# Kernel optimization log

Hardware: AMD Instinct MI355X
Metric: run time of the kernel (lower is better)

## Reference

```python
import jax, jax.numpy as jnp
import numpy as np

ROWS, COLS, P = 64, 64, 32
Q = 10                 # num_classes
TAU_EFF = 7
T1 = TAU_EFF + 1       # time bins
WRES = 3
WMAX = 2 ** WRES - 1   # 7
N = ROWS * COLS * P    # 131072 voter inputs


def setup_inputs() -> dict:
    key = jax.random.key(0)
    k_sp, _ = jax.random.split(key)
    # spike times in [0, tau_eff+2]; values >= tau_eff get clamped in forward
    input_spikes = jax.random.randint(k_sp, (ROWS, COLS, P), 0, TAU_EFF + 3).astype(jnp.float32)
    # w_init='half' -> wmax/2 everywhere
    weights = (WMAX / 2) * jnp.ones((2, N, Q, T1), dtype=jnp.float32)
    return {"input_spikes": input_spikes, "weights": weights}


def reference(input_spikes, weights):
    # flatten spikes: (rows, cols, p) -> (N,)
    v = input_spikes.reshape(-1)
    # clamp finite spike times >= tau_eff to tau_eff (Inf stays Inf)
    v = jnp.where((v >= TAU_EFF) & (v != jnp.inf), jnp.float32(TAU_EFF), v)
    # one-hot over time bins: equals torch's (const - voter_in) nonzero->-1, +1 trick.
    # Inf spike times produce all-zero rows (const - inf = -inf != 0), matching torch.
    const = jnp.arange(T1, dtype=jnp.float32)                       # (T1,)
    onehot = (const[None, None, None, :] == v[None, :, None, None]) # (2-broadcast later)
    voter_in = jnp.broadcast_to(onehot, (2, N, Q, T1)).astype(jnp.float32)
    # select weights at the spike-time bin; vote where selected weight >= wmax/2
    sel_weights = voter_in * weights                                # (2, N, Q, T1)
    votes = (sel_weights >= WMAX / 2).astype(jnp.float32)           # (2, N, Q, T1)
    # tally per class: sum over polarity, neurons, time bins
    tally = votes.sum(axis=(0, 1, 3))                               # (Q,)
    prediction = jnp.zeros((Q,), jnp.float32).at[jnp.argmax(tally)].set(1.0)
    return prediction, voter_in[0], votes
```

## Files before the change

### kernel.cpp

```cpp
#include <hip/hip_runtime.h>
#include <math.h>

#define NN      131072
#define Q       10
#define T1      8
#define GRID    2048
#define BLOCK   256

#define VIN0_OFF   10u
#define VIN0_SZ    (NN * Q * T1)
#define VOTES_OFF  (VIN0_OFF + VIN0_SZ)
#define VOTES_SZ   (2u * NN * Q * T1)
#define E_F2       (VOTES_SZ / 2u)

__global__ __launch_bounds__(BLOCK) void dtnn_main(
    const float* __restrict__ spikes,
    const float* __restrict__ weights,
    float* __restrict__ out,
    unsigned int* __restrict__ tallies)
{
    const unsigned int lane = threadIdx.x & 63u;
    const unsigned int wid  = threadIdx.x >> 6;

    float2* __restrict__ votes2 = (float2*)(out + VOTES_OFF);
    float2* __restrict__ vin2   = (float2*)(out + VIN0_OFF);

    unsigned int acc = 0u;

    const unsigned int stride = GRID * BLOCK;
    for (unsigned int j = blockIdx.x * BLOCK + threadIdx.x; j < E_F2; j += stride) {
        const unsigned int r    = j >> 2;
        const unsigned int slot = j & 3u;
        const unsigned int ri   = r / Q;
        const unsigned int q    = r - Q * ri;
        const unsigned int i    = ri & (NN - 1u);

        float v = spikes[i];
        v = (v >= 7.0f && !isinf(v)) ? 7.0f : v;
        const float t0 = (float)(2u * slot);
        const bool  h0 = (v == t0);
        const bool  h1 = (v == t0 + 1.0f);

        int tv = (int)v;
        tv = tv < 0 ? 0 : (tv > 7 ? 7 : tv);
        const float w  = weights[r * 8u + (unsigned)tv];
        const bool  gw = (w >= 3.5f);

        const float vx = (h0 && gw) ? 1.0f : 0.0f;
        const float vy = (h1 && gw) ? 1.0f : 0.0f;
        votes2[j] = make_float2(vx, vy);

        if (r < NN * Q) {
            vin2[j] = make_float2(h0 ? 1.0f : 0.0f, h1 ? 1.0f : 0.0f);
        }

        const bool inc = (vx != 0.0f) | (vy != 0.0f);
        #pragma unroll
        for (int k = 0; k < Q; ++k) {
            const unsigned long long m = __ballot(inc && (q == (unsigned)k));
            if (lane == (unsigned)k) acc += (unsigned)__popcll(m);
        }
    }

    __shared__ unsigned int lt[4 * Q];
    if (lane < Q) lt[wid * Q + lane] = acc;
    __syncthreads();
    if (threadIdx.x < Q) {
        tallies[threadIdx.x * GRID + blockIdx.x] =
            lt[threadIdx.x] + lt[Q + threadIdx.x] + lt[2 * Q + threadIdx.x] + lt[3 * Q + threadIdx.x];
    }
}

__global__ __launch_bounds__(64 * Q) void dtnn_pred(
    const unsigned int* __restrict__ tallies,
    float* __restrict__ out)
{
    const unsigned int lane = threadIdx.x & 63u;
    const unsigned int q    = threadIdx.x >> 6;

    unsigned int s = 0;
    #pragma unroll
    for (int it = 0; it < GRID / 64; ++it)
        s += tallies[q * GRID + it * 64 + lane];
    #pragma unroll
    for (int off = 32; off >= 1; off >>= 1)
        s += __shfl_down(s, off, 64);

    __shared__ unsigned int sums[Q];
    if (lane == 0) sums[q] = s;
    __syncthreads();

    if (threadIdx.x == 0) {
        unsigned int best = sums[0]; int bi = 0;
        #pragma unroll
        for (int k = 1; k < Q; ++k)
            if (sums[k] > best) { best = sums[k]; bi = k; }
        #pragma unroll
        for (int k = 0; k < Q; ++k) out[k] = (k == bi) ? 1.0f : 0.0f;
    }
}

extern "C" void kernel_launch(void* const* d_in, const int* in_sizes, int n_in,
                              void* d_out, int out_size, void* d_ws, size_t ws_size,
                              hipStream_t stream) {
    const float* spikes  = (const float*)d_in[0];
    const float* weights = (const float*)d_in[1];
    float* out = (float*)d_out;
    unsigned int* tallies = (unsigned int*)d_ws;

    dtnn_main<<<GRID, BLOCK, 0, stream>>>(spikes, weights, out, tallies);
    dtnn_pred<<<1, 64 * Q, 0, stream>>>(tallies, out);
}
```

Measured before the change: 43.87 us.

## Split vote computation into bitmask pass and separate output-writing pass

The fused kernel is split in two. The first pass does one gather per (polarity, neuron, class) row, packs the vote bits into a 64-bit ballot mask in workspace, and accumulates tallies. The second pass reads the compact mask to write the votes and voter_in arrays, using contiguous per-block chunks instead of a grid-stride loop. The goal is to take the scattered weight reads out of the store-bound output loop, at the cost of an extra kernel launch and a round trip of the mask through workspace.

```diff
diff --git a/kernel.cpp b/kernel.cpp
--- a/kernel.cpp
+++ b/kernel.cpp
@@ -12,53 +12,50 @@
 #define VOTES_OFF  (VIN0_OFF + VIN0_SZ)
 #define VOTES_SZ   (2u * NN * Q * T1)
 #define E_F2       (VOTES_SZ / 2u)
+#define CHUNK2     (E_F2 / GRID)
 
-__global__ __launch_bounds__(BLOCK) void dtnn_main(
+#define ROWS_T     (2u * NN * Q)
+#define CHUNK1     (ROWS_T / GRID)
+#define MASK_WORDS (ROWS_T / 64u)
+
+#define TALLY_BYTES (Q * GRID * 4)
+
+__global__ __launch_bounds__(BLOCK) void dtnn_pass1(
     const float* __restrict__ spikes,
     const float* __restrict__ weights,
-    float* __restrict__ out,
+    unsigned long long* __restrict__ mask,
     unsigned int* __restrict__ tallies)
 {
     const unsigned int lane = threadIdx.x & 63u;
     const unsigned int wid  = threadIdx.x >> 6;
 
-    float2* __restrict__ votes2 = (float2*)(out + VOTES_OFF);
-    float2* __restrict__ vin2   = (float2*)(out + VIN0_OFF);
-
     unsigned int acc = 0u;
 
-    const unsigned int stride = GRID * BLOCK;
-    for (unsigned int j = blockIdx.x * BLOCK + threadIdx.x; j < E_F2; j += stride) {
-        const unsigned int r    = j >> 2;
-        const unsigned int slot = j & 3u;
-        const unsigned int ri   = r / Q;
-        const unsigned int q    = r - Q * ri;
-        const unsigned int i    = ri & (NN - 1u);
+    const unsigned int row_base = blockIdx.x * CHUNK1 + threadIdx.x;
+    #pragma unroll 1
+    for (unsigned int it = 0; it < CHUNK1 / BLOCK; ++it) {
+        const unsigned int row = row_base + it * BLOCK;
+        const unsigned int ri  = row / Q;
+        const unsigned int q   = row - Q * ri;
+        const unsigned int i   = ri & (NN - 1u);
 
         float v = spikes[i];
-        v = (v >= 7.0f && !isinf(v)) ? 7.0f : v;
-        const float t0 = (float)(2u * slot);
-        const bool  h0 = (v == t0);
-        const bool  h1 = (v == t0 + 1.0f);
+        if (v >= 7.0f && !isinf(v)) v = 7.0f;
+        const int  tv    = (int)v;
+        const bool valid = (v >= 0.0f) && (v < 8.0f) && ((float)tv == v);
 
-        int tv = (int)v;
-        tv = tv < 0 ? 0 : (tv > 7 ? 7 : tv);
-        const float w  = weights[r * 8u + (unsigned)tv];
-        const bool  gw = (w >= 3.5f);
-
-        const float vx = (h0 && gw) ? 1.0f : 0.0f;
-        const float vy = (h1 && gw) ? 1.0f : 0.0f;
-        votes2[j] = make_float2(vx, vy);
-
-        if (r < NN * Q) {
-            vin2[j] = make_float2(h0 ? 1.0f : 0.0f, h1 ? 1.0f : 0.0f);
+        bool vote = false;
+        if (valid) {
+            vote = (weights[row * 8u + (unsigned)tv] >= 3.5f);
         }
 
-        const bool inc = (vx != 0.0f) | (vy != 0.0f);
+        const unsigned long long m = __ballot(vote);
+        if (lane == 0) mask[row >> 6] = m;
+
         #pragma unroll
         for (int k = 0; k < Q; ++k) {
-            const unsigned long long m = __ballot(inc && (q == (unsigned)k));
-            if (lane == (unsigned)k) acc += (unsigned)__popcll(m);
+            const unsigned long long mk = __ballot(vote && (q == (unsigned)k));
+            if (lane == (unsigned)k) acc += (unsigned)__popcll(mk);
         }
     }
 
@@ -68,6 +65,40 @@
     if (threadIdx.x < Q) {
         tallies[threadIdx.x * GRID + blockIdx.x] =
             lt[threadIdx.x] + lt[Q + threadIdx.x] + lt[2 * Q + threadIdx.x] + lt[3 * Q + threadIdx.x];
+    }
+}
+
+__global__ __launch_bounds__(BLOCK) void dtnn_pass2(
+    const float* __restrict__ spikes,
+    const unsigned long long* __restrict__ mask,
+    float* __restrict__ out)
+{
+    float2* __restrict__ votes2 = (float2*)(out + VOTES_OFF);
+    float2* __restrict__ vin2   = (float2*)(out + VIN0_OFF);
+
+    const unsigned int jbase = blockIdx.x * CHUNK2 + threadIdx.x;
+    #pragma unroll 1
+    for (unsigned int it = 0; it < CHUNK2 / BLOCK; ++it) {
+        const unsigned int j    = jbase + it * BLOCK;
+        const unsigned int r    = j >> 2;
+        const unsigned int slot = j & 3u;
+        const unsigned int ri   = r / Q;
+        const unsigned int i    = ri & (NN - 1u);
+
+        float v = spikes[i];
+        if (v >= 7.0f && !isinf(v)) v = 7.0f;
+        const float t0 = (float)(2u * slot);
+        const bool  h0 = (v == t0);
+        const bool  h1 = (v == t0 + 1.0f);
+
+        const bool bit = (mask[r >> 6] >> (r & 63u)) & 1ull;
+
+        votes2[j] = make_float2((h0 && bit) ? 1.0f : 0.0f,
+                                (h1 && bit) ? 1.0f : 0.0f);
+
+        if (r < NN * Q) {
+            vin2[j] = make_float2(h0 ? 1.0f : 0.0f, h1 ? 1.0f : 0.0f);
+        }
     }
 }
 
@@ -106,8 +137,10 @@
     const float* spikes  = (const float*)d_in[0];
     const float* weights = (const float*)d_in[1];
     float* out = (float*)d_out;
-    unsigned int* tallies = (unsigned int*)d_ws;
+    unsigned int*       tallies = (unsigned int*)d_ws;
+    unsigned long long* mask    = (unsigned long long*)((char*)d_ws + TALLY_BYTES);
 
-    dtnn_main<<<GRID, BLOCK, 0, stream>>>(spikes, weights, out, tallies);
+    dtnn_pass1<<<GRID, BLOCK, 0, stream>>>(spikes, weights, mask, tallies);
+    dtnn_pass2<<<GRID, BLOCK, 0, stream>>>(spikes, mask, out);
     dtnn_pred<<<1, 64 * Q, 0, stream>>>(tallies, out);
 }
```

After: 42.18 us. 1.04x faster.

## Widen output stores to aligned float4 with peeled head/tail elements

Applied to the files above, without the earlier changes.

The output buffer offset (10 floats) makes float4 stores misaligned, so the kernel shifts by two floats and writes aligned float4 body chunks. One thread handles the leading and trailing float2 pieces separately. Each thread now covers 4 time bins that may straddle two rows, so it loads weights only when a spike hits its bins and counts up to two votes. Work per block is a fixed chunk instead of a grid-stride loop. This aims to halve store instructions and skip needless weight loads, at the cost of more complex index logic and divergence.

```diff
diff --git a/kernel.cpp b/kernel.cpp
--- a/kernel.cpp
+++ b/kernel.cpp
@@ -1,7 +1,7 @@
 #include <hip/hip_runtime.h>
 #include <math.h>
 
-#define NN      131072
+#define NN      131072u
 #define Q       10
 #define T1      8
 #define GRID    2048
@@ -11,7 +11,15 @@
 #define VIN0_SZ    (NN * Q * T1)
 #define VOTES_OFF  (VIN0_OFF + VIN0_SZ)
 #define VOTES_SZ   (2u * NN * Q * T1)
-#define E_F2       (VOTES_SZ / 2u)
+#define ROWS_T     (2u * NN * Q)
+
+#define VBODY_N    ((VOTES_SZ - 4u) / 4u)
+#define VINBODY_N  ((VIN0_SZ  - 4u) / 4u)
+#define CH4        2560u
+
+__device__ __forceinline__ float clamp_spike(float v) {
+    return (v >= 7.0f && !isinf(v)) ? 7.0f : v;
+}
 
 __global__ __launch_bounds__(BLOCK) void dtnn_main(
     const float* __restrict__ spikes,
@@ -22,42 +30,87 @@
     const unsigned int lane = threadIdx.x & 63u;
     const unsigned int wid  = threadIdx.x >> 6;
 
-    float2* __restrict__ votes2 = (float2*)(out + VOTES_OFF);
-    float2* __restrict__ vin2   = (float2*)(out + VIN0_OFF);
+    float4* __restrict__ votes4 = (float4*)(out + VOTES_OFF + 2u);
+    float4* __restrict__ vin4   = (float4*)(out + VIN0_OFF + 2u);
 
     unsigned int acc = 0u;
 
-    const unsigned int stride = GRID * BLOCK;
-    for (unsigned int j = blockIdx.x * BLOCK + threadIdx.x; j < E_F2; j += stride) {
-        const unsigned int r    = j >> 2;
-        const unsigned int slot = j & 3u;
-        const unsigned int ri   = r / Q;
-        const unsigned int q    = r - Q * ri;
-        const unsigned int i    = ri & (NN - 1u);
+    if (blockIdx.x == 0) {
+        if (threadIdx.x == 0) {
+            const float v = clamp_spike(spikes[0]);
+            const bool h0 = (v == 0.0f), h1 = (v == 1.0f);
+            bool vote = false;
+            if (h0 | h1) vote = (weights[(unsigned)(int)v] >= 3.5f);
+            ((float2*)(out + VOTES_OFF))[0] =
+                make_float2((h0 && vote) ? 1.0f : 0.0f, (h1 && vote) ? 1.0f : 0.0f);
+            ((float2*)(out + VIN0_OFF))[0] =
+                make_float2(h0 ? 1.0f : 0.0f, h1 ? 1.0f : 0.0f);
+            acc += vote ? 1u : 0u;
+        }
+        if (threadIdx.x == 9) {
+            const unsigned rt = ROWS_T - 1u;
+            const float v = clamp_spike(spikes[(rt / Q) & (NN - 1u)]);
+            const bool h6 = (v == 6.0f), h7 = (v == 7.0f);
+            bool vote = false;
+            if (h6 | h7) vote = (weights[rt * 8u + (unsigned)(int)v] >= 3.5f);
+            ((float2*)(out + VOTES_OFF + VOTES_SZ - 2u))[0] =
+                make_float2((h6 && vote) ? 1.0f : 0.0f, (h7 && vote) ? 1.0f : 0.0f);
+            acc += vote ? 1u : 0u;
+            const unsigned rv = NN * Q - 1u;
+            const float v2 = clamp_spike(spikes[(rv / Q) & (NN - 1u)]);
+            ((float2*)(out + VIN0_OFF + VIN0_SZ - 2u))[0] =
+                make_float2((v2 == 6.0f) ? 1.0f : 0.0f, (v2 == 7.0f) ? 1.0f : 0.0f);
+        }
+    }
 
-        float v = spikes[i];
-        v = (v >= 7.0f && !isinf(v)) ? 7.0f : v;
-        const float t0 = (float)(2u * slot);
-        const bool  h0 = (v == t0);
-        const bool  h1 = (v == t0 + 1.0f);
-
-        int tv = (int)v;
-        tv = tv < 0 ? 0 : (tv > 7 ? 7 : tv);
-        const float w  = weights[r * 8u + (unsigned)tv];
-        const bool  gw = (w >= 3.5f);
-
-        const float vx = (h0 && gw) ? 1.0f : 0.0f;
-        const float vy = (h1 && gw) ? 1.0f : 0.0f;
-        votes2[j] = make_float2(vx, vy);
-
-        if (r < NN * Q) {
-            vin2[j] = make_float2(h0 ? 1.0f : 0.0f, h1 ? 1.0f : 0.0f);
+    const unsigned int jb = blockIdx.x * CH4 + threadIdx.x;
+    #pragma unroll 1
+    for (unsigned int it = 0; it < CH4 / BLOCK; ++it) {
+        const unsigned int b = jb + it * BLOCK;
+        bool inc1 = false, inc2 = false;
+        unsigned int qa = 0u, qb = 0u;
+        if (b < VBODY_N) {
+            const unsigned int f  = 4u * b + 2u;
+            const unsigned int r  = f >> 3;
+            const unsigned int ri = r / Q;
+            const unsigned int q  = r - Q * ri;
+            const unsigned int i  = ri & (NN - 1u);
+            const float v = clamp_spike(spikes[i]);
+            float4 vo, vi_;
+            qa = q;
+            if ((f & 4u) == 0u) {
+                const bool h2 = (v == 2.0f), h3 = (v == 3.0f), h4 = (v == 4.0f), h5 = (v == 5.0f);
+                bool vote = false;
+                if (h2 | h3 | h4 | h5) vote = (weights[r * 8u + (unsigned)(int)v] >= 3.5f);
+                vi_ = make_float4(h2 ? 1.0f : 0.0f, h3 ? 1.0f : 0.0f,
+                                  h4 ? 1.0f : 0.0f, h5 ? 1.0f : 0.0f);
+                vo  = make_float4((h2 && vote) ? 1.0f : 0.0f, (h3 && vote) ? 1.0f : 0.0f,
+                                  (h4 && vote) ? 1.0f : 0.0f, (h5 && vote) ? 1.0f : 0.0f);
+                inc1 = vote;
+            } else {
+                const bool h6 = (v == 6.0f), h7 = (v == 7.0f);
+                bool vote_a = false;
+                if (h6 | h7) vote_a = (weights[r * 8u + (unsigned)(int)v] >= 3.5f);
+                const bool wrap = (q == (unsigned)(Q - 1));
+                qb = wrap ? 0u : (q + 1u);
+                const unsigned int i1 = (ri + (wrap ? 1u : 0u)) & (NN - 1u);
+                const float v1 = clamp_spike(spikes[i1]);
+                const bool g0 = (v1 == 0.0f), g1 = (v1 == 1.0f);
+                bool vote_b = false;
+                if (g0 | g1) vote_b = (weights[(r + 1u) * 8u + (unsigned)(int)v1] >= 3.5f);
+                vi_ = make_float4(h6 ? 1.0f : 0.0f, h7 ? 1.0f : 0.0f,
+                                  g0 ? 1.0f : 0.0f, g1 ? 1.0f : 0.0f);
+                vo  = make_float4((h6 && vote_a) ? 1.0f : 0.0f, (h7 && vote_a) ? 1.0f : 0.0f,
+                                  (g0 && vote_b) ? 1.0f : 0.0f, (g1 && vote_b) ? 1.0f : 0.0f);
+                inc1 = vote_a; inc2 = vote_b;
+            }
+            votes4[b] = vo;
+            if (b < VINBODY_N) vin4[b] = vi_;
         }
-
-        const bool inc = (vx != 0.0f) | (vy != 0.0f);
         #pragma unroll
         for (int k = 0; k < Q; ++k) {
-            const unsigned long long m = __ballot(inc && (q == (unsigned)k));
+            const unsigned long long m =
+                __ballot((inc1 && qa == (unsigned)k) || (inc2 && qb == (unsigned)k));
             if (lane == (unsigned)k) acc += (unsigned)__popcll(m);
         }
     }
```

Measured after the change: 41.82 us. -4.7%, faster.
